# Optimization experiments

Measured on AMD Instinct MI355X. Metric: run time of the kernel, lower is better.

Reference implementation:

```python
import jax, jax.numpy as jnp
import numpy as np

B, H, W, C = 32, 56, 56, 256
NH, WS, SH = 8, 7, 3
HD = C // NH
SCALE = HD ** -0.5
N = WS * WS
MLP = 4 * C


def _rel_pos_index():
    coords = np.stack(np.meshgrid(np.arange(WS), np.arange(WS), indexing='ij')).reshape(2, -1)
    rel = (coords[:, :, None] - coords[:, None, :]).transpose(1, 2, 0)
    rel[..., 0] += WS - 1
    rel[..., 1] += WS - 1
    rel[..., 0] *= 2 * WS - 1
    return jnp.asarray(rel.sum(-1))  # (N, N) int


def _attn_mask():
    # standard Swin shifted-window mask, computed statically
    img = np.zeros((H, W))
    cnt = 0
    for hs in (slice(0, -WS), slice(-WS, -SH), slice(-SH, None)):
        for ws_ in (slice(0, -WS), slice(-WS, -SH), slice(-SH, None)):
            img[hs, ws_] = cnt
            cnt += 1
    mw = img.reshape(H // WS, WS, W // WS, WS).transpose(0, 2, 1, 3).reshape(-1, N)
    am = mw[:, None, :] - mw[:, :, None]
    am = np.where(am != 0, -1e9, 0.0).astype(np.float32)
    return jnp.asarray(am)  # (nW, N, N)


def _part(x):
    b = x.shape[0]
    x = x.reshape(b, H // WS, WS, W // WS, WS, C)
    return x.transpose(0, 1, 3, 2, 4, 5).reshape(-1, N, C)


def _rev(xw):
    x = xw.reshape(-1, H // WS, W // WS, WS, WS, C)
    return x.transpose(0, 1, 3, 2, 4, 5).reshape(-1, H, W, C)


def _ln(x, g, b):
    m = x.mean(-1, keepdims=True)
    v = x.var(-1, keepdims=True)
    return (x - m) / jnp.sqrt(v + 1e-5) * g + b


def setup_inputs() -> dict:
    key = jax.random.key(0)
    ks = jax.random.split(key, 6)
    s = 0.02
    return {
        'x': jax.random.normal(ks[0], (B, H, W, C), jnp.float32),
        'gamma1': jnp.ones((C,), jnp.float32),
        'beta1': jnp.zeros((C,), jnp.float32),
        'w_qkv': jax.random.normal(ks[1], (C, 3 * C), jnp.float32) * s,
        'b_qkv': jnp.zeros((3 * C,), jnp.float32),
        'rpb': jax.random.normal(ks[2], ((2 * WS - 1) ** 2, NH), jnp.float32) * s,
        'w_proj': jax.random.normal(ks[3], (C, C), jnp.float32) * s,
        'b_proj': jnp.zeros((C,), jnp.float32),
        'gamma2': jnp.ones((C,), jnp.float32),
        'beta2': jnp.zeros((C,), jnp.float32),
        'w_fc1': jax.random.normal(ks[4], (C, MLP), jnp.float32) * s,
        'b_fc1': jnp.zeros((MLP,), jnp.float32),
        'w_fc2': jax.random.normal(ks[5], (MLP, C), jnp.float32) * s,
        'b_fc2': jnp.zeros((C,), jnp.float32),
    }


def reference(x, gamma1, beta1, w_qkv, b_qkv, rpb, w_proj, b_proj, gamma2, beta2, w_fc1, b_fc1, w_fc2, b_fc2):
    idx = _rel_pos_index()
    mask = _attn_mask()  # (nW, N, N)
    nW = mask.shape[0]

    shortcut = x
    xn = _ln(x, gamma1, beta1)
    xs = jnp.roll(xn, (-SH, -SH), axis=(1, 2))        # cyclic shift
    xw = _part(xs)                                     # (B*nW, N, C)

    qkv = (xw @ w_qkv + b_qkv).reshape(-1, N, 3, NH, HD).transpose(2, 0, 3, 1, 4)
    # SNN-variant IF (ReLU) gates on q, k, v
    q, k, v = jax.nn.relu(qkv[0]), jax.nn.relu(qkv[1]), jax.nn.relu(qkv[2])

    attn = jnp.einsum('bhnd,bhmd->bhnm', q * SCALE, k)  # (B*nW, NH, N, N)
    bias = rpb[idx].transpose(2, 0, 1)                  # (NH, N, N)
    attn = attn + bias[None]
    attn = attn.reshape(-1, nW, NH, N, N) + mask[None, :, None]
    attn = attn.reshape(-1, NH, N, N)
    # stdp_qk ReLU before softmax (faithful to source)
    attn = jax.nn.softmax(jax.nn.relu(attn), axis=-1)
    # stdp_av ReLU on attention output
    out = jax.nn.relu(jnp.einsum('bhnm,bhmd->bhnd', attn, v))
    out = out.transpose(0, 2, 1, 3).reshape(-1, N, C) @ w_proj + b_proj

    xs = _rev(out)
    x = shortcut + jnp.roll(xs, (SH, SH), axis=(1, 2))  # reverse shift + residual

    h = jax.nn.gelu(_ln(x, gamma2, beta2) @ w_fc1 + b_fc1, approximate=False)
    return x + h @ w_fc2 + b_fc2
```

## Files before the change

kernel.cpp:

```cpp
#include <hip/hip_runtime.h>
#include <stdint.h>

typedef unsigned short u16;
typedef short bf16x8 __attribute__((ext_vector_type(8)));
typedef float f32x4 __attribute__((ext_vector_type(4)));

#define NTOK 100352
#define NWIN 2048
#define CC 256
#define NHEAD 8
#define HDIM 32
#define NWT 49
#define MLPD 1024
#define ATT_SCALE 0.17677669529663687f

__device__ __forceinline__ u16 f2b(float f) {
  union { float f; uint32_t u; } c; c.f = f;
  return (u16)((c.u + 0x7fffu + ((c.u >> 16) & 1u)) >> 16);
}
__device__ __forceinline__ float b2f(u16 h) {
  union { uint32_t u; float f; } c; c.u = ((uint32_t)h) << 16;
  return c.f;
}

__device__ __forceinline__ void gload_lds16(const void* g, void* l) {
  __builtin_amdgcn_global_load_lds((const __attribute__((address_space(1))) void*)g,
                                   (__attribute__((address_space(3))) void*)l, 16, 0, 0);
}

__global__ __launch_bounds__(256) void wconv_k(const float* __restrict__ w,
                                               u16* __restrict__ wT, int K, int N) {
  int i = blockIdx.x * 256 + threadIdx.x;
  if (i < K * N) {
    int k = i / N, n = i % N;
    wT[(size_t)n * K + k] = f2b(w[i]);
  }
}

__global__ __launch_bounds__(256) void bias_lut_k(const float* __restrict__ rpb,
                                                  float* __restrict__ lut) {
  int i = blockIdx.x * 256 + threadIdx.x;
  if (i >= 8 * 64 * 64) return;
  int h = i >> 12, m = (i >> 6) & 63, n = i & 63;
  float v = 0.f;
  if (m < 49 && n < 49) {
    int i1 = n / 7, j1 = n % 7;
    int i2 = m / 7, j2 = m % 7;
    v = rpb[((i1 - i2 + 6) * 13 + (j1 - j2 + 6)) * 8 + h];
  }
  lut[i] = v;
}

template<bool PART>
__global__ __launch_bounds__(256)
void ln_k(const float* __restrict__ x, const float* __restrict__ g,
          const float* __restrict__ be, u16* __restrict__ out) {
  int token = blockIdx.x * 4 + (threadIdx.x >> 6);
  int lane = threadIdx.x & 63;
  size_t src;
  if (PART) {
    int win = token / 49, nn = token % 49;
    int b = win >> 6, wh = (win >> 3) & 7, ww = win & 7;
    int i = nn / 7, j = nn % 7;
    int h = wh * 7 + i + 3; if (h >= 56) h -= 56;
    int w = ww * 7 + j + 3; if (w >= 56) w -= 56;
    src = ((size_t)((b * 56 + h) * 56 + w)) * CC;
  } else {
    src = (size_t)token * CC;
  }
  f32x4 v = *(const f32x4*)&x[src + lane * 4];
  float s1 = v[0] + v[1] + v[2] + v[3];
  float s2 = v[0]*v[0] + v[1]*v[1] + v[2]*v[2] + v[3]*v[3];
#pragma unroll
  for (int o = 32; o; o >>= 1) { s1 += __shfl_xor(s1, o); s2 += __shfl_xor(s2, o); }
  float mean = s1 * (1.f / 256.f);
  float var = s2 * (1.f / 256.f) - mean * mean;
  float rstd = rsqrtf(var + 1e-5f);
  f32x4 gv = *(const f32x4*)&g[lane * 4];
  f32x4 bv = *(const f32x4*)&be[lane * 4];
  float y0 = (v[0]-mean)*rstd*gv[0] + bv[0];
  float y1 = (v[1]-mean)*rstd*gv[1] + bv[1];
  float y2 = (v[2]-mean)*rstd*gv[2] + bv[2];
  float y3 = (v[3]-mean)*rstd*gv[3] + bv[3];
  uint32_t lo = f2b(y0) | ((uint32_t)f2b(y1) << 16);
  uint32_t hi = f2b(y2) | ((uint32_t)f2b(y3) << 16);
  *(uint2*)&out[(size_t)token * CC + lane * 4] = make_uint2(lo, hi);
}

#define BM 128
#define BN 128
#define BK 64
enum { EPI_QKV = 0, EPI_PROJ = 1, EPI_GELU = 2, EPI_FC2 = 3 };

template<int EPI, int NKT>
__global__ __launch_bounds__(256)
void gemm_k(const u16* __restrict__ A, const u16* __restrict__ BT,
            const float* __restrict__ bias,
            void* __restrict__ p0, const void* __restrict__ p1) {
  constexpr int K = NKT * BK;
  __shared__ u16 aL[2][BM * BK];
  __shared__ u16 bL[2][BN * BK];
  const int tid = threadIdx.x;
  const int lane = tid & 63;
  const int wv = tid >> 6;
  const int wm = wv >> 1, wn = wv & 1;

  int bx = blockIdx.x, by = blockIdx.y;
  {
    int nwg = gridDim.x * gridDim.y;
    int lin = by * gridDim.x + bx;
    int q = nwg >> 3, r = nwg & 7;
    int xcd = lin & 7, idx = lin >> 3;
    int wg = (xcd < r ? xcd * (q + 1) : r * (q + 1) + (xcd - r) * q) + idx;
    bx = wg % gridDim.x;
    by = wg / gridDim.x;
  }
  const long m0 = (long)by * BM;
  const int n0 = bx * BN;

  f32x4 acc[4][4] = {};
  const int r15 = lane & 15;
  const int g4 = lane >> 4;

  const u16* pA[4];
  const u16* pB[4];
  int lslot[4];
#pragma unroll
  for (int it = 0; it < 4; ++it) {
    int slot = tid + 256 * it;
    int row = slot >> 3, c8 = slot & 7;
    int cs = c8 ^ (row & 7);
    pA[it] = &A[(m0 + row) * K + cs * 8];
    pB[it] = &BT[(size_t)(n0 + row) * K + cs * 8];
    lslot[it] = slot * 8;
  }
  int aoff[2][4], boff[2][4];
#pragma unroll
  for (int kk = 0; kk < 2; ++kk)
#pragma unroll
    for (int m = 0; m < 4; ++m) {
      int rowa = wm * 64 + m * 16 + r15;
      aoff[kk][m] = rowa * BK + (((kk * 4 + g4) ^ (rowa & 7)) << 3);
      int rowb = wn * 64 + m * 16 + r15;
      boff[kk][m] = rowb * BK + (((kk * 4 + g4) ^ (rowb & 7)) << 3);
    }

  auto stage = [&](int bufi) {
#pragma unroll
    for (int it = 0; it < 4; ++it) { gload_lds16(pA[it], &aL[bufi][lslot[it]]); pA[it] += BK; }
#pragma unroll
    for (int it = 0; it < 4; ++it) { gload_lds16(pB[it], &bL[bufi][lslot[it]]); pB[it] += BK; }
  };

  stage(0);
  stage(1);

#pragma unroll
  for (int t = 0; t < NKT; ++t) {
    if (t + 1 < NKT) asm volatile("s_waitcnt vmcnt(8)" ::: "memory");
    else             asm volatile("s_waitcnt vmcnt(0)" ::: "memory");
    __builtin_amdgcn_sched_barrier(0);
    __builtin_amdgcn_s_barrier();
    __builtin_amdgcn_sched_barrier(0);
    {
      const u16* ab = aL[t & 1];
      const u16* bb = bL[t & 1];
#pragma unroll
      for (int kk = 0; kk < 2; ++kk) {
        bf16x8 af[4], bfr[4];
#pragma unroll
        for (int m = 0; m < 4; ++m) af[m] = *(const bf16x8*)&ab[aoff[kk][m]];
#pragma unroll
        for (int n = 0; n < 4; ++n) bfr[n] = *(const bf16x8*)&bb[boff[kk][n]];
#pragma unroll
        for (int n = 0; n < 4; ++n)
#pragma unroll
          for (int m = 0; m < 4; ++m)
            acc[n][m] = __builtin_amdgcn_mfma_f32_16x16x32_bf16(bfr[n], af[m], acc[n][m], 0, 0, 0);
      }
    }
    __builtin_amdgcn_sched_barrier(0);
    __builtin_amdgcn_s_barrier();
    __builtin_amdgcn_sched_barrier(0);
    if (t + 2 < NKT) stage(t & 1);
  }

#pragma unroll
  for (int mt = 0; mt < 4; ++mt) {
    const int mrow = (int)m0 + wm * 64 + mt * 16 + r15;
    int win = 0, nn = 0;
    size_t pix = 0;
    if (EPI == EPI_QKV || EPI == EPI_PROJ) {
      win = mrow / 49; nn = mrow - win * 49;
      if (EPI == EPI_PROJ) {
        int b = win >> 6, wh = (win >> 3) & 7, ww = win & 7;
        int i = nn / 7, jj = nn - i * 7;
        int h = wh * 7 + i + 3; if (h >= 56) h -= 56;
        int w = ww * 7 + jj + 3; if (w >= 56) w -= 56;
        pix = (size_t)((b * 56 + h) * 56 + w);
      }
    }
#pragma unroll
    for (int nt = 0; nt < 4; ++nt) {
      const int col0 = n0 + wn * 64 + nt * 16 + g4 * 4;
      f32x4 bv = *(const f32x4*)&bias[col0];
      f32x4 v;
#pragma unroll
      for (int j = 0; j < 4; ++j) v[j] = acc[nt][mt][j] + bv[j];
      if (EPI == EPI_QKV) {
        int s = col0 >> 8, head = (col0 >> 5) & 7, d0 = col0 & 31;
        float sc = (s == 0) ? ATT_SCALE : 1.f;
#pragma unroll
        for (int j = 0; j < 4; ++j) v[j] = fmaxf(v[j], 0.f) * sc;
        uint32_t w0 = (uint32_t)f2b(v[0]) | ((uint32_t)f2b(v[1]) << 16);
        uint32_t w1 = (uint32_t)f2b(v[2]) | ((uint32_t)f2b(v[3]) << 16);
        u16* dst = (u16*)p0 + (size_t)s * ((size_t)NTOK * CC);
        *(uint2*)&dst[(((size_t)(win * NHEAD + head)) * NWT + nn) * HDIM + d0] =
            make_uint2(w0, w1);
      } else if (EPI == EPI_PROJ) {
        f32x4 r = *(const f32x4*)&((const float*)p1)[pix * CC + col0];
#pragma unroll
        for (int j = 0; j < 4; ++j) v[j] += r[j];
        *(f32x4*)&((float*)p0)[pix * CC + col0] = v;
      } else if (EPI == EPI_GELU) {
#pragma unroll
        for (int j = 0; j < 4; ++j)
          v[j] = 0.5f * v[j] * (1.f + erff(v[j] * 0.70710678118654752f));
        uint32_t w0 = (uint32_t)f2b(v[0]) | ((uint32_t)f2b(v[1]) << 16);
        uint32_t w1 = (uint32_t)f2b(v[2]) | ((uint32_t)f2b(v[3]) << 16);
        *(uint2*)&((u16*)p0)[(size_t)mrow * MLPD + col0] = make_uint2(w0, w1);
      } else {
        size_t idx = (size_t)mrow * CC + col0;
        f32x4 r = *(const f32x4*)&((const float*)p1)[idx];
#pragma unroll
        for (int j = 0; j < 4; ++j) v[j] += r[j];
        *(f32x4*)&((float*)p0)[idx] = v;
      }
    }
  }
}

__global__ __launch_bounds__(256)
void attn_mfma_k(const u16* __restrict__ q, const u16* __restrict__ k2,
                 const u16* __restrict__ v2, const float* __restrict__ lut,
                 u16* __restrict__ out) {
  __shared__ u16 P_lds[4][64 * 72];
  const int tid = threadIdx.x;
  const int wv = tid >> 6;
  const int lane = tid & 63;
  const int c = lane & 15;
  const int g = lane >> 4;
  const int blk = blockIdx.x * 4 + wv;
  const int head = blk & 7;
  const int win = blk >> 3;
  const int wimg = win & 63;
  const int wh = wimg >> 3, ww = wimg & 7;
  const size_t base = (size_t)blk * (NWT * HDIM);
  u16* Pw = P_lds[wv];

  bf16x8 kf[4], qf[4];
#pragma unroll
  for (int t = 0; t < 4; ++t) {
    kf[t] = *(const bf16x8*)&k2[base + (size_t)(t * 16 + c) * HDIM + g * 8];
    qf[t] = *(const bf16x8*)&q [base + (size_t)(t * 16 + c) * HDIM + g * 8];
  }
  bf16x8 vf[2][2];
#pragma unroll
  for (int kcc = 0; kcc < 2; ++kcc)
#pragma unroll
    for (int td = 0; td < 2; ++td)
#pragma unroll
      for (int jj = 0; jj < 8; ++jj) {
        int m = kcc * 32 + g * 8 + jj;
        m = m < 49 ? m : 48;
        vf[kcc][td][jj] = (short)v2[base + (size_t)m * HDIM + td * 16 + c];
      }

  f32x4 acc[4][4] = {};
#pragma unroll
  for (int tm = 0; tm < 4; ++tm)
#pragma unroll
    for (int tn = 0; tn < 4; ++tn)
      acc[tm][tn] = __builtin_amdgcn_mfma_f32_16x16x32_bf16(kf[tm], qf[tn], acc[tm][tn], 0, 0, 0);

  const float* lrow = &lut[(size_t)head * 64 * 64];
  int Ln[4];
#pragma unroll
  for (int tn = 0; tn < 4; ++tn) {
    int n = tn * 16 + c;
    int i1 = (n * 9363) >> 16;
    int j1 = n - i1 * 7;
    int rh = (wh < 7) ? 0 : (i1 < 4 ? 1 : 2);
    int rw = (ww < 7) ? 0 : (j1 < 4 ? 1 : 2);
    Ln[tn] = rh * 3 + rw;
  }
  float colmax[4] = {0.f, 0.f, 0.f, 0.f};
#pragma unroll
  for (int tm = 0; tm < 4; ++tm)
#pragma unroll
    for (int j = 0; j < 4; ++j) {
      int m = tm * 16 + g * 4 + j;
      int i2 = (m * 9363) >> 16;
      int j2 = m - i2 * 7;
      int rh = (wh < 7) ? 0 : (i2 < 4 ? 1 : 2);
      int rw = (ww < 7) ? 0 : (j2 < 4 ? 1 : 2);
      int Lm = rh * 3 + rw;
#pragma unroll
      for (int tn = 0; tn < 4; ++tn) {
        float s = acc[tm][tn][j] + lrow[m * 64 + tn * 16 + c];
        s = fmaxf(s, 0.f);
        if (Lm != Ln[tn]) s = 0.f;
        acc[tm][tn][j] = s;
        colmax[tn] = fmaxf(colmax[tn], s);
      }
    }
#pragma unroll
  for (int tn = 0; tn < 4; ++tn) {
    colmax[tn] = fmaxf(colmax[tn], __shfl_xor(colmax[tn], 16));
    colmax[tn] = fmaxf(colmax[tn], __shfl_xor(colmax[tn], 32));
  }
  float colsum[4] = {0.f, 0.f, 0.f, 0.f};
#pragma unroll
  for (int tm = 0; tm < 4; ++tm)
#pragma unroll
    for (int j = 0; j < 4; ++j) {
      int m = tm * 16 + g * 4 + j;
      bool mvalid = (m < NWT);
#pragma unroll
      for (int tn = 0; tn < 4; ++tn) {
        float e = mvalid ? __expf(acc[tm][tn][j] - colmax[tn]) : 0.f;
        acc[tm][tn][j] = e;
        colsum[tn] += e;
      }
    }
#pragma unroll
  for (int tn = 0; tn < 4; ++tn) {
    colsum[tn] += __shfl_xor(colsum[tn], 16);
    colsum[tn] += __shfl_xor(colsum[tn], 32);
    colsum[tn] = 1.f / colsum[tn];
  }

#pragma unroll
  for (int tn = 0; tn < 4; ++tn) {
    int n = tn * 16 + c;
#pragma unroll
    for (int tm = 0; tm < 4; ++tm) {
      float r = colsum[tn];
      uint32_t w0 = (uint32_t)f2b(acc[tm][tn][0] * r) | ((uint32_t)f2b(acc[tm][tn][1] * r) << 16);
      uint32_t w1 = (uint32_t)f2b(acc[tm][tn][2] * r) | ((uint32_t)f2b(acc[tm][tn][3] * r) << 16);
      *(uint2*)&Pw[n * 72 + tm * 16 + g * 4] = make_uint2(w0, w1);
    }
  }

  f32x4 oacc[4][2] = {};
#pragma unroll
  for (int kcc = 0; kcc < 2; ++kcc) {
    bf16x8 pf[4];
#pragma unroll
    for (int tr = 0; tr < 4; ++tr)
      pf[tr] = *(const bf16x8*)&Pw[(tr * 16 + c) * 72 + kcc * 32 + g * 8];
#pragma unroll
    for (int tr = 0; tr < 4; ++tr)
#pragma unroll
      for (int td = 0; td < 2; ++td)
        oacc[tr][td] = __builtin_amdgcn_mfma_f32_16x16x32_bf16(pf[tr], vf[kcc][td], oacc[tr][td], 0, 0, 0);
  }

#pragma unroll
  for (int tr = 0; tr < 4; ++tr)
#pragma unroll
    for (int j = 0; j < 4; ++j) {
      int n = tr * 16 + g * 4 + j;
      if (n < NWT) {
#pragma unroll
        for (int td = 0; td < 2; ++td) {
          int d = td * 16 + c;
          out[((size_t)(win * NWT + n)) * CC + head * HDIM + d] =
              f2b(fmaxf(oacc[tr][td][j], 0.f));
        }
      }
    }
}

extern "C" void kernel_launch(void* const* d_in, const int* in_sizes, int n_in,
                              void* d_out, int out_size, void* d_ws, size_t ws_size,
                              hipStream_t stream) {
  const float* x      = (const float*)d_in[0];
  const float* gamma1 = (const float*)d_in[1];
  const float* beta1  = (const float*)d_in[2];
  const float* w_qkv  = (const float*)d_in[3];
  const float* b_qkv  = (const float*)d_in[4];
  const float* rpb    = (const float*)d_in[5];
  const float* w_proj = (const float*)d_in[6];
  const float* b_proj = (const float*)d_in[7];
  const float* gamma2 = (const float*)d_in[8];
  const float* beta2  = (const float*)d_in[9];
  const float* w_fc1  = (const float*)d_in[10];
  const float* b_fc1  = (const float*)d_in[11];
  const float* w_fc2  = (const float*)d_in[12];
  const float* b_fc2  = (const float*)d_in[13];
  float* out = (float*)d_out;

  char* ws = (char*)d_ws;
  size_t off = 0;
  auto alloc = [&](size_t bytes) { void* p = ws + off; off = (off + bytes + 255) & ~(size_t)255; return p; };

  u16* wqkvT = (u16*)alloc(768 * 256 * 2);
  u16* wprojT = (u16*)alloc(256 * 256 * 2);
  u16* wfc1T = (u16*)alloc(1024 * 256 * 2);
  u16* wfc2T = (u16*)alloc(256 * 1024 * 2);
  float* lut = (float*)alloc(8 * 64 * 64 * 4);
  u16* region2 = (u16*)alloc((size_t)NTOK * CC * 2);
  char* region1 = (char*)alloc((size_t)3 * NTOK * CC * 2);

  u16* xw = region2;
  u16* qb = (u16*)region1;
  u16* kb = qb + (size_t)NTOK * CC;
  u16* vb = kb + (size_t)NTOK * CC;
  u16* attn_out = region2;
  float* x2 = (float*)region1;
  u16* xn2 = region2;
  u16* hbuf = (u16*)(region1 + (size_t)NTOK * CC * 4);

  if (ws_size < off) return;

  wconv_k<<<(256 * 768 + 255) / 256, 256, 0, stream>>>(w_qkv, wqkvT, 256, 768);
  wconv_k<<<(256 * 256 + 255) / 256, 256, 0, stream>>>(w_proj, wprojT, 256, 256);
  wconv_k<<<(256 * 1024 + 255) / 256, 256, 0, stream>>>(w_fc1, wfc1T, 256, 1024);
  wconv_k<<<(1024 * 256 + 255) / 256, 256, 0, stream>>>(w_fc2, wfc2T, 1024, 256);
  bias_lut_k<<<(8 * 64 * 64) / 256, 256, 0, stream>>>(rpb, lut);

  ln_k<true><<<NTOK / 4, 256, 0, stream>>>(x, gamma1, beta1, xw);

  gemm_k<EPI_QKV, 4><<<dim3(768 / BN, NTOK / BM), 256, 0, stream>>>(
      xw, wqkvT, b_qkv, (void*)qb, nullptr);

  attn_mfma_k<<<NWIN * NHEAD / 4, 256, 0, stream>>>(qb, kb, vb, lut, attn_out);

  gemm_k<EPI_PROJ, 4><<<dim3(256 / BN, NTOK / BM), 256, 0, stream>>>(
      attn_out, wprojT, b_proj, (void*)x2, (const void*)x);

  ln_k<false><<<NTOK / 4, 256, 0, stream>>>(x2, gamma2, beta2, xn2);

  const int MCH = 25088;
  for (int c = 0; c < 4; ++c) {
    const u16* a1 = xn2 + (size_t)c * MCH * CC;
    gemm_k<EPI_GELU, 4><<<dim3(MLPD / BN, MCH / BM), 256, 0, stream>>>(
        a1, wfc1T, b_fc1, (void*)hbuf, nullptr);
    gemm_k<EPI_FC2, 16><<<dim3(CC / BN, MCH / BM), 256, 0, stream>>>(
        hbuf, wfc2T, b_fc2, (void*)(out + (size_t)c * MCH * CC),
        (const void*)(x2 + (size_t)c * MCH * CC));
  }
}
```

Baseline: 516.6 us.

## Fuse proj GEMM with residual and LayerNorm2, merge prep kernels, cheaper GELU

Replaces the projection GEMM and the separate second LayerNorm with one 256x256-tile kernel that adds bias and residual, reduces row statistics across waves through LDS, and writes both x2 and normalized bf16 output. This removes a full read/write pass over the activations and a launch. It also merges the weight-conversion and bias-LUT kernels into one launch, uses the packed v_cvt_pk_bf16_f32 instruction for conversions, and swaps erf GELU for the tanh approximation. The larger tile gives fewer blocks and heavy LDS use, which may reduce occupancy, and the tanh GELU slightly changes numerics.

```diff
diff --git a/kernel.cpp b/kernel.cpp
--- a/kernel.cpp
+++ b/kernel.cpp
@@ -22,52 +22,59 @@
   union { uint32_t u; float f; } c; c.u = ((uint32_t)h) << 16;
   return c.f;
 }
+__device__ __forceinline__ uint32_t f2b2(float lo, float hi) {
+  uint32_t r;
+  asm("v_cvt_pk_bf16_f32 %0, %1, %2" : "=v"(r) : "v"(lo), "v"(hi));
+  return r;
+}
 
 __device__ __forceinline__ void gload_lds16(const void* g, void* l) {
   __builtin_amdgcn_global_load_lds((const __attribute__((address_space(1))) void*)g,
                                    (__attribute__((address_space(3))) void*)l, 16, 0, 0);
 }
 
-__global__ __launch_bounds__(256) void wconv_k(const float* __restrict__ w,
-                                               u16* __restrict__ wT, int K, int N) {
+__global__ __launch_bounds__(256)
+void prep_k(const float* __restrict__ wqkv, const float* __restrict__ wproj,
+            const float* __restrict__ wfc1, const float* __restrict__ wfc2,
+            const float* __restrict__ rpb,
+            u16* __restrict__ qkvT, u16* __restrict__ projT,
+            u16* __restrict__ fc1T, u16* __restrict__ fc2T, float* __restrict__ lut) {
   int i = blockIdx.x * 256 + threadIdx.x;
-  if (i < K * N) {
-    int k = i / N, n = i % N;
-    wT[(size_t)n * K + k] = f2b(w[i]);
-  }
-}
-
-__global__ __launch_bounds__(256) void bias_lut_k(const float* __restrict__ rpb,
-                                                  float* __restrict__ lut) {
-  int i = blockIdx.x * 256 + threadIdx.x;
-  if (i >= 8 * 64 * 64) return;
-  int h = i >> 12, m = (i >> 6) & 63, n = i & 63;
-  float v = 0.f;
-  if (m < 49 && n < 49) {
-    int i1 = n / 7, j1 = n % 7;
-    int i2 = m / 7, j2 = m % 7;
-    v = rpb[((i1 - i2 + 6) * 13 + (j1 - j2 + 6)) * 8 + h];
-  }
-  lut[i] = v;
-}
-
-template<bool PART>
+  if (i < 196608) {
+    int k = i / 768, n = i % 768;
+    qkvT[(size_t)n * 256 + k] = f2b(wqkv[i]);
+  } else if (i < 262144) {
+    int j = i - 196608, k = j / 256, n = j % 256;
+    projT[(size_t)n * 256 + k] = f2b(wproj[j]);
+  } else if (i < 524288) {
+    int j = i - 262144, k = j / 1024, n = j % 1024;
+    fc1T[(size_t)n * 256 + k] = f2b(wfc1[j]);
+  } else if (i < 786432) {
+    int j = i - 524288, k = j / 256, n = j % 256;
+    fc2T[(size_t)n * 1024 + k] = f2b(wfc2[j]);
+  } else if (i < 819200) {
+    int j = i - 786432;
+    int h = j >> 12, m = (j >> 6) & 63, n = j & 63;
+    float v = 0.f;
+    if (m < 49 && n < 49) {
+      int i1 = n / 7, j1 = n % 7, i2 = m / 7, j2 = m % 7;
+      v = rpb[((i1 - i2 + 6) * 13 + (j1 - j2 + 6)) * 8 + h];
+    }
+    lut[j] = v;
+  }
+}
+
 __global__ __launch_bounds__(256)
 void ln_k(const float* __restrict__ x, const float* __restrict__ g,
           const float* __restrict__ be, u16* __restrict__ out) {
   int token = blockIdx.x * 4 + (threadIdx.x >> 6);
   int lane = threadIdx.x & 63;
-  size_t src;
-  if (PART) {
-    int win = token / 49, nn = token % 49;
-    int b = win >> 6, wh = (win >> 3) & 7, ww = win & 7;
-    int i = nn / 7, j = nn % 7;
-    int h = wh * 7 + i + 3; if (h >= 56) h -= 56;
-    int w = ww * 7 + j + 3; if (w >= 56) w -= 56;
-    src = ((size_t)((b * 56 + h) * 56 + w)) * CC;
-  } else {
-    src = (size_t)token * CC;
-  }
+  int win = token / 49, nn = token % 49;
+  int b = win >> 6, wh = (win >> 3) & 7, ww = win & 7;
+  int i = nn / 7, j = nn % 7;
+  int h = wh * 7 + i + 3; if (h >= 56) h -= 56;
+  int w = ww * 7 + j + 3; if (w >= 56) w -= 56;
+  size_t src = ((size_t)((b * 56 + h) * 56 + w)) * CC;
   f32x4 v = *(const f32x4*)&x[src + lane * 4];
   float s1 = v[0] + v[1] + v[2] + v[3];
   float s2 = v[0]*v[0] + v[1]*v[1] + v[2]*v[2] + v[3]*v[3];
@@ -82,15 +89,13 @@
   float y1 = (v[1]-mean)*rstd*gv[1] + bv[1];
   float y2 = (v[2]-mean)*rstd*gv[2] + bv[2];
   float y3 = (v[3]-mean)*rstd*gv[3] + bv[3];
-  uint32_t lo = f2b(y0) | ((uint32_t)f2b(y1) << 16);
-  uint32_t hi = f2b(y2) | ((uint32_t)f2b(y3) << 16);
-  *(uint2*)&out[(size_t)token * CC + lane * 4] = make_uint2(lo, hi);
+  *(uint2*)&out[(size_t)token * CC + lane * 4] = make_uint2(f2b2(y0, y1), f2b2(y2, y3));
 }
 
 #define BM 128
 #define BN 128
 #define BK 64
-enum { EPI_QKV = 0, EPI_PROJ = 1, EPI_GELU = 2, EPI_FC2 = 3 };
+enum { EPI_QKV = 0, EPI_GELU = 2, EPI_FC2 = 3 };
 
 template<int EPI, int NKT>
 __global__ __launch_bounds__(256)
@@ -189,17 +194,7 @@
   for (int mt = 0; mt < 4; ++mt) {
     const int mrow = (int)m0 + wm * 64 + mt * 16 + r15;
     int win = 0, nn = 0;
-    size_t pix = 0;
-    if (EPI == EPI_QKV || EPI == EPI_PROJ) {
-      win = mrow / 49; nn = mrow - win * 49;
-      if (EPI == EPI_PROJ) {
-        int b = win >> 6, wh = (win >> 3) & 7, ww = win & 7;
-        int i = nn / 7, jj = nn - i * 7;
-        int h = wh * 7 + i + 3; if (h >= 56) h -= 56;
-        int w = ww * 7 + jj + 3; if (w >= 56) w -= 56;
-        pix = (size_t)((b * 56 + h) * 56 + w);
-      }
-    }
+    if (EPI == EPI_QKV) { win = mrow / 49; nn = mrow - win * 49; }
 #pragma unroll
     for (int nt = 0; nt < 4; ++nt) {
       const int col0 = n0 + wn * 64 + nt * 16 + g4 * 4;
@@ -212,23 +207,18 @@
         float sc = (s == 0) ? ATT_SCALE : 1.f;
 #pragma unroll
         for (int j = 0; j < 4; ++j) v[j] = fmaxf(v[j], 0.f) * sc;
-        uint32_t w0 = (uint32_t)f2b(v[0]) | ((uint32_t)f2b(v[1]) << 16);
-        uint32_t w1 = (uint32_t)f2b(v[2]) | ((uint32_t)f2b(v[3]) << 16);
         u16* dst = (u16*)p0 + (size_t)s * ((size_t)NTOK * CC);
         *(uint2*)&dst[(((size_t)(win * NHEAD + head)) * NWT + nn) * HDIM + d0] =
-            make_uint2(w0, w1);
-      } else if (EPI == EPI_PROJ) {
-        f32x4 r = *(const f32x4*)&((const float*)p1)[pix * CC + col0];
-#pragma unroll
-        for (int j = 0; j < 4; ++j) v[j] += r[j];
-        *(f32x4*)&((float*)p0)[pix * CC + col0] = v;
+            make_uint2(f2b2(v[0], v[1]), f2b2(v[2], v[3]));
       } else if (EPI == EPI_GELU) {
 #pragma unroll
-        for (int j = 0; j < 4; ++j)
-          v[j] = 0.5f * v[j] * (1.f + erff(v[j] * 0.70710678118654752f));
-        uint32_t w0 = (uint32_t)f2b(v[0]) | ((uint32_t)f2b(v[1]) << 16);
-        uint32_t w1 = (uint32_t)f2b(v[2]) | ((uint32_t)f2b(v[3]) << 16);
-        *(uint2*)&((u16*)p0)[(size_t)mrow * MLPD + col0] = make_uint2(w0, w1);
+        for (int j = 0; j < 4; ++j) {
+          float u = 0.79788456f * (v[j] + 0.044715f * v[j] * v[j] * v[j]);
+          float th = 1.f - 2.f / (__expf(2.f * u) + 1.f);
+          v[j] = 0.5f * v[j] * (1.f + th);
+        }
+        *(uint2*)&((u16*)p0)[(size_t)mrow * MLPD + col0] =
+            make_uint2(f2b2(v[0], v[1]), f2b2(v[2], v[3]));
       } else {
         size_t idx = (size_t)mrow * CC + col0;
         f32x4 r = *(const f32x4*)&((const float*)p1)[idx];
@@ -236,6 +226,158 @@
         for (int j = 0; j < 4; ++j) v[j] += r[j];
         *(f32x4*)&((float*)p0)[idx] = v;
       }
+    }
+  }
+}
+
+__global__ __launch_bounds__(512)
+void gemm_ln_k(const u16* __restrict__ A, const u16* __restrict__ BT,
+               const float* __restrict__ bias, const float* __restrict__ xres,
+               const float* __restrict__ g2, const float* __restrict__ be2,
+               float* __restrict__ x2, u16* __restrict__ xn2) {
+  constexpr int K = 256;
+  __shared__ u16 aL[2][256 * 64];
+  __shared__ u16 bL[2][256 * 64];
+  const int tid = threadIdx.x;
+  const int lane = tid & 63;
+  const int wv = tid >> 6;
+  const int wm = wv >> 1;
+  const int wn = wv & 1;
+  const int r15 = lane & 15;
+  const int g4 = lane >> 4;
+
+  int by = blockIdx.x;
+  {
+    int nwg = gridDim.x;
+    int q = nwg >> 3, r = nwg & 7;
+    int xcd = by & 7, idx = by >> 3;
+    by = (xcd < r ? xcd * (q + 1) : r * (q + 1) + (xcd - r) * q) + idx;
+  }
+  const long m0 = (long)by * 256;
+
+  f32x4 acc[8][4] = {};
+
+  const u16* pA[4];
+  const u16* pB[4];
+  int lslot[4];
+#pragma unroll
+  for (int it = 0; it < 4; ++it) {
+    int slot = tid + 512 * it;
+    int row = slot >> 3, c8 = slot & 7;
+    int cs = c8 ^ (row & 7);
+    pA[it] = &A[(m0 + row) * K + cs * 8];
+    pB[it] = &BT[(size_t)row * K + cs * 8];
+    lslot[it] = slot * 8;
+  }
+  int aoff[2][4], boff[2][8];
+#pragma unroll
+  for (int kk = 0; kk < 2; ++kk) {
+#pragma unroll
+    for (int m = 0; m < 4; ++m) {
+      int rowa = wm * 64 + m * 16 + r15;
+      aoff[kk][m] = rowa * BK + (((kk * 4 + g4) ^ (rowa & 7)) << 3);
+    }
+#pragma unroll
+    for (int n = 0; n < 8; ++n) {
+      int rowb = wn * 128 + n * 16 + r15;
+      boff[kk][n] = rowb * BK + (((kk * 4 + g4) ^ (rowb & 7)) << 3);
+    }
+  }
+
+  auto stage = [&](int bufi) {
+#pragma unroll
+    for (int it = 0; it < 4; ++it) { gload_lds16(pA[it], &aL[bufi][lslot[it]]); pA[it] += BK; }
+#pragma unroll
+    for (int it = 0; it < 4; ++it) { gload_lds16(pB[it], &bL[bufi][lslot[it]]); pB[it] += BK; }
+  };
+
+  stage(0);
+  stage(1);
+
+#pragma unroll
+  for (int t = 0; t < 4; ++t) {
+    if (t + 1 < 4) asm volatile("s_waitcnt vmcnt(8)" ::: "memory");
+    else           asm volatile("s_waitcnt vmcnt(0)" ::: "memory");
+    __builtin_amdgcn_sched_barrier(0);
+    __builtin_amdgcn_s_barrier();
+    __builtin_amdgcn_sched_barrier(0);
+    {
+      const u16* ab = aL[t & 1];
+      const u16* bb = bL[t & 1];
+#pragma unroll
+      for (int kk = 0; kk < 2; ++kk) {
+        bf16x8 af[4], bfr[8];
+#pragma unroll
+        for (int m = 0; m < 4; ++m) af[m] = *(const bf16x8*)&ab[aoff[kk][m]];
+#pragma unroll
+        for (int n = 0; n < 8; ++n) bfr[n] = *(const bf16x8*)&bb[boff[kk][n]];
+#pragma unroll
+        for (int n = 0; n < 8; ++n)
+#pragma unroll
+          for (int m = 0; m < 4; ++m)
+            acc[n][m] = __builtin_amdgcn_mfma_f32_16x16x32_bf16(bfr[n], af[m], acc[n][m], 0, 0, 0);
+      }
+    }
+    __builtin_amdgcn_sched_barrier(0);
+    __builtin_amdgcn_s_barrier();
+    __builtin_amdgcn_sched_barrier(0);
+    if (t + 2 < 4) stage(t & 1);
+  }
+
+  float* st = (float*)&aL[0][0];
+  size_t pix[4];
+  float s1[4] = {}, s2[4] = {};
+#pragma unroll
+  for (int mt = 0; mt < 4; ++mt) {
+    const int mrow = (int)m0 + wm * 64 + mt * 16 + r15;
+    int win = mrow / 49, nn = mrow - win * 49;
+    int b = win >> 6, wh = (win >> 3) & 7, ww = win & 7;
+    int i = nn / 7, jj = nn - i * 7;
+    int h = wh * 7 + i + 3; if (h >= 56) h -= 56;
+    int w = ww * 7 + jj + 3; if (w >= 56) w -= 56;
+    pix[mt] = (size_t)((b * 56 + h) * 56 + w);
+#pragma unroll
+    for (int nt = 0; nt < 8; ++nt) {
+      const int col0 = wn * 128 + nt * 16 + g4 * 4;
+      f32x4 bv = *(const f32x4*)&bias[col0];
+      f32x4 r = *(const f32x4*)&xres[pix[mt] * CC + col0];
+      f32x4 v;
+#pragma unroll
+      for (int j = 0; j < 4; ++j) {
+        v[j] = acc[nt][mt][j] + bv[j] + r[j];
+        s1[mt] += v[j];
+        s2[mt] += v[j] * v[j];
+      }
+      *(f32x4*)&x2[pix[mt] * CC + col0] = v;
+      acc[nt][mt] = v;
+    }
+    s1[mt] += __shfl_xor(s1[mt], 16);  s1[mt] += __shfl_xor(s1[mt], 32);
+    s2[mt] += __shfl_xor(s2[mt], 16);  s2[mt] += __shfl_xor(s2[mt], 32);
+    if (g4 == 0) {
+      int wrow = wm * 64 + mt * 16 + r15;
+      st[(wn * 256 + wrow) * 2 + 0] = s1[mt];
+      st[(wn * 256 + wrow) * 2 + 1] = s2[mt];
+    }
+  }
+  __syncthreads();
+#pragma unroll
+  for (int mt = 0; mt < 4; ++mt) {
+    int wrow = wm * 64 + mt * 16 + r15;
+    float t1 = s1[mt] + st[((wn ^ 1) * 256 + wrow) * 2 + 0];
+    float t2 = s2[mt] + st[((wn ^ 1) * 256 + wrow) * 2 + 1];
+    float mean = t1 * (1.f / 256.f);
+    float var = t2 * (1.f / 256.f) - mean * mean;
+    float rstd = rsqrtf(var + 1e-5f);
+#pragma unroll
+    for (int nt = 0; nt < 8; ++nt) {
+      const int col0 = wn * 128 + nt * 16 + g4 * 4;
+      f32x4 gv = *(const f32x4*)&g2[col0];
+      f32x4 bv = *(const f32x4*)&be2[col0];
+      float y0 = (acc[nt][mt][0] - mean) * rstd * gv[0] + bv[0];
+      float y1 = (acc[nt][mt][1] - mean) * rstd * gv[1] + bv[1];
+      float y2 = (acc[nt][mt][2] - mean) * rstd * gv[2] + bv[2];
+      float y3 = (acc[nt][mt][3] - mean) * rstd * gv[3] + bv[3];
+      *(uint2*)&xn2[pix[mt] * CC + col0] = make_uint2(f2b2(y0, y1), f2b2(y2, y3));
     }
   }
 }
@@ -346,9 +488,9 @@
 #pragma unroll
     for (int tm = 0; tm < 4; ++tm) {
       float r = colsum[tn];
-      uint32_t w0 = (uint32_t)f2b(acc[tm][tn][0] * r) | ((uint32_t)f2b(acc[tm][tn][1] * r) << 16);
-      uint32_t w1 = (uint32_t)f2b(acc[tm][tn][2] * r) | ((uint32_t)f2b(acc[tm][tn][3] * r) << 16);
-      *(uint2*)&Pw[n * 72 + tm * 16 + g * 4] = make_uint2(w0, w1);
+      *(uint2*)&Pw[n * 72 + tm * 16 + g * 4] =
+          make_uint2(f2b2(acc[tm][tn][0] * r, acc[tm][tn][1] * r),
+                     f2b2(acc[tm][tn][2] * r, acc[tm][tn][3] * r));
     }
   }
 
@@ -419,28 +561,23 @@
   u16* vb = kb + (size_t)NTOK * CC;
   u16* attn_out = region2;
   float* x2 = (float*)region1;
-  u16* xn2 = region2;
-  u16* hbuf = (u16*)(region1 + (size_t)NTOK * CC * 4);
+  u16* xn2 = (u16*)(region1 + (size_t)NTOK * CC * 4);
+  u16* hbuf = region2;
 
   if (ws_size < off) return;
 
-  wconv_k<<<(256 * 768 + 255) / 256, 256, 0, stream>>>(w_qkv, wqkvT, 256, 768);
-  wconv_k<<<(256 * 256 + 255) / 256, 256, 0, stream>>>(w_proj, wprojT, 256, 256);
-  wconv_k<<<(256 * 1024 + 255) / 256, 256, 0, stream>>>(w_fc1, wfc1T, 256, 1024);
-  wconv_k<<<(1024 * 256 + 255) / 256, 256, 0, stream>>>(w_fc2, wfc2T, 1024, 256);
-  bias_lut_k<<<(8 * 64 * 64) / 256, 256, 0, stream>>>(rpb, lut);
-
-  ln_k<true><<<NTOK / 4, 256, 0, stream>>>(x, gamma1, beta1, xw);
+  prep_k<<<3200, 256, 0, stream>>>(w_qkv, w_proj, w_fc1, w_fc2, rpb,
+                                   wqkvT, wprojT, wfc1T, wfc2T, lut);
+
+  ln_k<<<NTOK / 4, 256, 0, stream>>>(x, gamma1, beta1, xw);
 
   gemm_k<EPI_QKV, 4><<<dim3(768 / BN, NTOK / BM), 256, 0, stream>>>(
       xw, wqkvT, b_qkv, (void*)qb, nullptr);
 
   attn_mfma_k<<<NWIN * NHEAD / 4, 256, 0, stream>>>(qb, kb, vb, lut, attn_out);
 
-  gemm_k<EPI_PROJ, 4><<<dim3(256 / BN, NTOK / BM), 256, 0, stream>>>(
-      attn_out, wprojT, b_proj, (void*)x2, (const void*)x);
-
-  ln_k<false><<<NTOK / 4, 256, 0, stream>>>(x2, gamma2, beta2, xn2);
+  gemm_ln_k<<<NTOK / 256, 512, 0, stream>>>(
+      attn_out, wprojT, b_proj, x, gamma2, beta2, x2, xn2);
 
   const int MCH = 25088;
   for (int c = 0; c < 4; ++c) {
```

Result: no change. 514.2 us (-0.5%).
